# Kernel optimization log

Measured on AMD Instinct MI355X. Metric: run time of the kernel, lower is better.

Reference implementation:

```python
import jax, jax.numpy as jnp
import numpy as np

GRID = 14
N_HEADS = 12
TOP_K = 32


def _valid_indices(grid):
    """Replicates create_locality_mask: cls row/col always valid; patch pairs
    valid iff Chebyshev distance on the grid <= 2 (includes diagonal)."""
    n = grid * grid + 1
    mask = np.zeros((n, n), dtype=bool)
    mask[0, :] = True
    mask[:, 0] = True
    idx = np.arange(grid * grid)
    r, c = idx // grid, idx % grid
    cheb = np.maximum(np.abs(r[:, None] - r[None, :]), np.abs(c[:, None] - c[None, :]))
    mask[1:, 1:] = cheb <= 2
    i_idx, j_idx = np.nonzero(mask)
    return jnp.asarray(i_idx, dtype=jnp.int32), jnp.asarray(j_idx, dtype=jnp.int32)

I_IDX, J_IDX = _valid_indices(GRID)  # nv = 4489 valid (query, key) pairs


def setup_inputs() -> dict:
    key = jax.random.key(0)
    ks = jax.random.split(key, 6)
    B, L, D = 32, GRID * GRID + 1, 768
    s = 0.02
    return {
        "x": jax.random.normal(ks[0], (B, L, D), jnp.float32),
        "W_q": jax.random.normal(ks[1], (D, D), jnp.float32) * s,
        "b_q": jnp.zeros((D,), jnp.float32),
        "W_k": jax.random.normal(ks[2], (D, D), jnp.float32) * s,
        "b_k": jnp.zeros((D,), jnp.float32),
        "W_v": jax.random.normal(ks[3], (D, D), jnp.float32) * s,
        "b_v": jnp.zeros((D,), jnp.float32),
        "W_o": jax.random.normal(ks[4], (D, D), jnp.float32) * s,
        "b_o": jnp.zeros((D,), jnp.float32),
        "log_sigma": jnp.zeros((), jnp.float32),  # sigma = 1.0
    }


def reference(x, W_q, b_q, W_k, b_k, W_v, b_v, W_o, b_o, log_sigma):
    B, L, D = x.shape
    H, dk = N_HEADS, D // N_HEADS

    def proj(W, b):
        y = jnp.einsum('bld,de->ble', x, W) + b
        return y.reshape(B, L, H, dk).transpose(0, 2, 1, 3)  # [B,H,L,dk]

    Q, K, V = proj(W_q, b_q), proj(W_k, b_k), proj(W_v, b_v)

    sigma_sq = jnp.exp(2.0 * log_sigma)
    # gather valid (i,j) pairs; nv pairs from the locality mask
    q_valid = Q[:, :, I_IDX, :]                       # [B,H,nv,dk]
    k_valid = K[:, :, J_IDX, :]                       # [B,H,nv,dk]
    dist_sq = jnp.sum((q_valid - k_valid) ** 2, axis=-1)  # [B,H,nv]
    scores_valid = (-0.5 / sigma_sq) * dist_sq

    neg_inf = jnp.array(-jnp.inf, x.dtype)
    scores = jnp.full((B, H, L, L), neg_inf, dtype=x.dtype)
    scores = scores.at[:, :, I_IDX, J_IDX].set(scores_valid)

    k_top = min(TOP_K, L)
    _, top_idx = jax.lax.top_k(scores, k_top)          # [B,H,L,k]
    bb = jnp.arange(B)[:, None, None, None]
    hh = jnp.arange(H)[None, :, None, None]
    nn = jnp.arange(L)[None, None, :, None]
    topk_mask = jnp.zeros((B, H, L, L), bool).at[bb, hh, nn, top_idx].set(True)

    final_mask = jnp.isfinite(scores) & topk_mask
    scores = jnp.where(final_mask, scores, neg_inf)
    weights = jax.nn.softmax(scores, axis=-1)          # [B,H,L,L]
    attention_mask = (weights > 1e-6).astype(x.dtype)

    consensus = jnp.einsum('bhij,bhjd->bhid', weights, V)
    consensus = consensus.transpose(0, 2, 1, 3).reshape(B, L, D)
    out = jnp.einsum('bld,de->ble', consensus, W_o) + b_o
    return out, weights, attention_mask
```

## Files before the change

### kernel.cpp

```cpp
#include <hip/hip_runtime.h>
#include <hip/hip_bf16.h>
#include <math.h>

#define GRIDN 14
#define L 197
#define H 12
#define DK 64
#define D 768
#define B 32
#define BL (B*L)
#define TOPK 32
#define NBH (B*H)
#define NROW (NBH*L)
#define QKV_ELEMS ((size_t)NROW*DK)
#define KSTR 68
#define KROWS 127

typedef __attribute__((ext_vector_type(8))) short short8;
typedef __attribute__((ext_vector_type(4))) float floatx4;

__device__ __forceinline__ void load_lds16(void* lds, const void* g) {
    __builtin_amdgcn_global_load_lds(
        (const __attribute__((address_space(1))) unsigned int*)g,
        (__attribute__((address_space(3))) unsigned int*)lds, 16, 0, 0);
}

__global__ __launch_bounds__(256)
void prep(const float* __restrict__ x,
          const float* __restrict__ Wq, const float* __restrict__ Wk,
          const float* __restrict__ Wv, const float* __restrict__ Wo,
          __hip_bfloat16* __restrict__ xh, __hip_bfloat16* __restrict__ xl,
          __hip_bfloat16* __restrict__ WqTh, __hip_bfloat16* __restrict__ WqTl,
          __hip_bfloat16* __restrict__ WkTh, __hip_bfloat16* __restrict__ WkTl,
          __hip_bfloat16* __restrict__ WvT,  __hip_bfloat16* __restrict__ WoT)
{
    const int z = blockIdx.z;
    if (z == 4) {
        int lin = (blockIdx.y * 24 + blockIdx.x) * 256 + threadIdx.x;
        for (int i = lin; i < BL * D / 4; i += 24 * 24 * 256) {
            float4 v = ((const float4*)x)[i];
            union { __hip_bfloat16 b[4]; short4 s; } hh, ll;
            float f[4] = {v.x, v.y, v.z, v.w};
            #pragma unroll
            for (int j = 0; j < 4; ++j) {
                __hip_bfloat16 h = __float2bfloat16(f[j]);
                hh.b[j] = h;
                ll.b[j] = __float2bfloat16(f[j] - __bfloat162float(h));
            }
            ((short4*)xh)[i] = hh.s;
            ((short4*)xl)[i] = ll.s;
        }
        return;
    }
    __shared__ float tile[32][33];
    const float* src = (z == 0) ? Wq : (z == 1) ? Wk : (z == 2) ? Wv : Wo;
    __hip_bfloat16* dh = (z == 0) ? WqTh : (z == 1) ? WkTh : (z == 2) ? WvT : WoT;
    __hip_bfloat16* dl = (z == 0) ? WqTl : (z == 1) ? WkTl : nullptr;
    const int k0 = blockIdx.y * 32, n0 = blockIdx.x * 32;
    const int tx = threadIdx.x & 31, ty = threadIdx.x >> 5;

    for (int r = ty; r < 32; r += 8)
        tile[r][tx] = src[(size_t)(k0 + r) * D + n0 + tx];
    __syncthreads();
    for (int r = ty; r < 32; r += 8) {
        float v = tile[tx][r];
        __hip_bfloat16 h = __float2bfloat16(v);
        dh[(size_t)(n0 + r) * D + k0 + tx] = h;
        if (dl) dl[(size_t)(n0 + r) * D + k0 + tx] =
            __float2bfloat16(v - __bfloat162float(h));
    }
}

__global__ __launch_bounds__(256)
void gemm_qkv(const __hip_bfloat16* __restrict__ xh, const __hip_bfloat16* __restrict__ xl,
              const __hip_bfloat16* __restrict__ Wqh, const __hip_bfloat16* __restrict__ Wql,
              const __hip_bfloat16* __restrict__ Wkh, const __hip_bfloat16* __restrict__ Wkl,
              const __hip_bfloat16* __restrict__ Wvh,
              const float* __restrict__ bq, const float* __restrict__ bk,
              const float* __restrict__ bv,
              float* __restrict__ Qb, float* __restrict__ Kb, float* __restrict__ Vb)
{
    __shared__ __attribute__((aligned(16))) __hip_bfloat16 Ash[128 * 32];
    __shared__ __attribute__((aligned(16))) __hip_bfloat16 Bsh[128 * 32];
    __shared__ __attribute__((aligned(16))) __hip_bfloat16 Asl[128 * 32];
    __shared__ __attribute__((aligned(16))) __hip_bfloat16 Bsl[128 * 32];

    const int grp = blockIdx.y / 6, nt = blockIdx.y % 6;
    const __hip_bfloat16 *Bth, *Btl; const float* bias; float* C;
    if (grp == 0)      { Bth = Wqh; Btl = Wql; bias = bq; C = Qb; }
    else if (grp == 1) { Bth = Wkh; Btl = Wkl; bias = bk; C = Kb; }
    else               { Bth = Wvh; Btl = nullptr; bias = bv; C = Vb; }
    const bool split = (grp < 2);

    const int tid = threadIdx.x;
    const int wave = tid >> 6, lane = tid & 63;
    const int quad = lane >> 4, l16 = lane & 15;
    const int m0 = blockIdx.x * 128, n0 = nt * 128;
    const int wm = (wave & 1) * 64, wn = (wave >> 1) * 64;

    floatx4 acc[4][4] = {};

    int s_r[2], s_cs[2];
    #pragma unroll
    for (int u = 0; u < 2; ++u) {
        int idx = tid + u * 256;
        s_r[u] = idx >> 2; s_cs[u] = idx & 3;
    }

    for (int k0 = 0; k0 < D; k0 += 32) {
        #pragma unroll
        for (int u = 0; u < 2; ++u) {
            int r = s_r[u];
            int csrc = s_cs[u] ^ ((r >> 1) & 3);
            int gm = m0 + r; if (gm >= BL) gm = BL - 1;
            size_t aoff = (size_t)gm * D + k0 + csrc * 8;
            size_t boff = (size_t)(n0 + r) * D + k0 + csrc * 8;
            int lds_off = (wave * 64 + u * 256) * 16;
            load_lds16((char*)Ash + lds_off, xh + aoff);
            load_lds16((char*)Bsh + lds_off, Bth + boff);
            if (split) {
                load_lds16((char*)Asl + lds_off, xl + aoff);
                load_lds16((char*)Bsl + lds_off, Btl + boff);
            }
        }
        __syncthreads();

        short8 ah[4], bh[4];
        #pragma unroll
        for (int a = 0; a < 4; ++a) {
            int r = wm + a * 16 + l16;
            int slot = (r << 2) + (quad ^ ((r >> 1) & 3));
            ah[a] = *(const short8*)((const char*)Ash + (slot << 4));
        }
        #pragma unroll
        for (int b2 = 0; b2 < 4; ++b2) {
            int r = wn + b2 * 16 + l16;
            int slot = (r << 2) + (quad ^ ((r >> 1) & 3));
            bh[b2] = *(const short8*)((const char*)Bsh + (slot << 4));
        }
        if (split) {
            short8 al[4], bl[4];
            #pragma unroll
            for (int a = 0; a < 4; ++a) {
                int r = wm + a * 16 + l16;
                int slot = (r << 2) + (quad ^ ((r >> 1) & 3));
                al[a] = *(const short8*)((const char*)Asl + (slot << 4));
            }
            #pragma unroll
            for (int b2 = 0; b2 < 4; ++b2) {
                int r = wn + b2 * 16 + l16;
                int slot = (r << 2) + (quad ^ ((r >> 1) & 3));
                bl[b2] = *(const short8*)((const char*)Bsl + (slot << 4));
            }
            #pragma unroll
            for (int a = 0; a < 4; ++a)
                #pragma unroll
                for (int b2 = 0; b2 < 4; ++b2) {
                    acc[a][b2] = __builtin_amdgcn_mfma_f32_16x16x32_bf16(
                        al[a], bh[b2], acc[a][b2], 0, 0, 0);
                    acc[a][b2] = __builtin_amdgcn_mfma_f32_16x16x32_bf16(
                        ah[a], bl[b2], acc[a][b2], 0, 0, 0);
                }
        }
        #pragma unroll
        for (int a = 0; a < 4; ++a)
            #pragma unroll
            for (int b2 = 0; b2 < 4; ++b2)
                acc[a][b2] = __builtin_amdgcn_mfma_f32_16x16x32_bf16(
                    ah[a], bh[b2], acc[a][b2], 0, 0, 0);
        __syncthreads();
    }

    #pragma unroll
    for (int b2 = 0; b2 < 4; ++b2) {
        int n = n0 + wn + b2 * 16 + l16;
        float bvv = bias[n];
        int hh = n >> 6, dd = n & 63;
        #pragma unroll
        for (int a = 0; a < 4; ++a) {
            #pragma unroll
            for (int r = 0; r < 4; ++r) {
                int m = m0 + wm + a * 16 + quad * 4 + r;
                if (m < BL) {
                    int bb = m / L, ll = m % L;
                    C[((((size_t)bb * H + hh) * L + ll) << 6) + dd] =
                        acc[a][b2][r] + bvv;
                }
            }
        }
    }
}

__global__ __launch_bounds__(256)
void gemm_o(const __hip_bfloat16* __restrict__ A,
            const __hip_bfloat16* __restrict__ Bt,
            const float* __restrict__ bias, float* __restrict__ C)
{
    __shared__ __attribute__((aligned(16))) __hip_bfloat16 As[128 * 32];
    __shared__ __attribute__((aligned(16))) __hip_bfloat16 Bts[128 * 32];

    const int tid = threadIdx.x;
    const int wave = tid >> 6, lane = tid & 63;
    const int quad = lane >> 4, l16 = lane & 15;
    const int m0 = blockIdx.x * 128, n0 = blockIdx.y * 128;
    const int wm = (wave & 1) * 64, wn = (wave >> 1) * 64;

    floatx4 acc[4][4] = {};

    int s_r[2], s_cs[2];
    #pragma unroll
    for (int u = 0; u < 2; ++u) {
        int idx = tid + u * 256;
        s_r[u] = idx >> 2; s_cs[u] = idx & 3;
    }

    for (int k0 = 0; k0 < D; k0 += 32) {
        #pragma unroll
        for (int u = 0; u < 2; ++u) {
            int r = s_r[u];
            int csrc = s_cs[u] ^ ((r >> 1) & 3);
            int gm = m0 + r; if (gm >= BL) gm = BL - 1;
            int lds_off = (wave * 64 + u * 256) * 16;
            load_lds16((char*)As + lds_off, A + (size_t)gm * D + k0 + csrc * 8);
            load_lds16((char*)Bts + lds_off, Bt + (size_t)(n0 + r) * D + k0 + csrc * 8);
        }
        __syncthreads();

        short8 af[4], bf[4];
        #pragma unroll
        for (int a = 0; a < 4; ++a) {
            int r = wm + a * 16 + l16;
            int slot = (r << 2) + (quad ^ ((r >> 1) & 3));
            af[a] = *(const short8*)((const char*)As + (slot << 4));
        }
        #pragma unroll
        for (int b2 = 0; b2 < 4; ++b2) {
            int r = wn + b2 * 16 + l16;
            int slot = (r << 2) + (quad ^ ((r >> 1) & 3));
            bf[b2] = *(const short8*)((const char*)Bts + (slot << 4));
        }
        #pragma unroll
        for (int a = 0; a < 4; ++a)
            #pragma unroll
            for (int b2 = 0; b2 < 4; ++b2)
                acc[a][b2] = __builtin_amdgcn_mfma_f32_16x16x32_bf16(
                    af[a], bf[b2], acc[a][b2], 0, 0, 0);
        __syncthreads();
    }

    #pragma unroll
    for (int b2 = 0; b2 < 4; ++b2) {
        int n = n0 + wn + b2 * 16 + l16;
        float bvv = bias[n];
        #pragma unroll
        for (int a = 0; a < 4; ++a) {
            #pragma unroll
            for (int r = 0; r < 4; ++r) {
                int m = m0 + wm + a * 16 + quad * 4 + r;
                if (m < BL) C[(size_t)m * D + n] = acc[a][b2][r] + bvv;
            }
        }
    }
}

__global__ __launch_bounds__(512)
void attn_fused(const float* __restrict__ Q, const float* __restrict__ Kg,
                const float* __restrict__ Vg, const float* __restrict__ logsig,
                float* __restrict__ wout, float* __restrict__ mout,
                __hip_bfloat16* __restrict__ cons)
{
    __shared__ __attribute__((aligned(16))) float KV[KROWS * KSTR];
    __shared__ float qbuf[8][64];
    __shared__ float clsbuf[L];
    __shared__ float wjW[99][32];
    __shared__ unsigned char wjJ[99][32];
    __shared__ unsigned int winA[L];
    __shared__ unsigned char joff[76];

    const int bh = blockIdx.x;
    const int yb = blockIdx.y;
    const int b = bh / H, h = bh % H;
    const int tid = threadIdx.x, wave = tid >> 6, lane = tid & 63;
    const int base_i = yb * 99;
    const int half = lane & 1;
    const int joffs = yb ? 70 : 0;

    if (tid >= 1 && tid < L) {
        int r = (tid - 1) / GRIDN, c = (tid - 1) % GRIDN;
        int r0 = r - 2 < 0 ? 0 : r - 2, r1 = r + 2 > 13 ? 13 : r + 2;
        int c0 = c - 2 < 0 ? 0 : c - 2, c1 = c + 2 > 13 ? 13 : c + 2;
        int Wd = c1 - c0 + 1, Hh = r1 - r0 + 1;
        winA[tid] = (unsigned)r0 | ((unsigned)c0 << 8) |
                    ((unsigned)Wd << 16) | ((unsigned)Hh << 24);
    }
    if (tid == 0) winA[0] = 0;
    if (tid < 75) {
        int w = tid / 25 + 3, tm = tid % 25;
        joff[tid] = (unsigned char)((tm / w) * GRIDN + tm % w);
    }

    int pr4[4], pc4[4];
    #pragma unroll
    for (int k = 0; k < 4; ++k) {
        int p = lane + (k << 6);
        if (p >= 1 && p < L) { pr4[k] = (p - 1) / GRIDN; pc4[k] = (p - 1) % GRIDN; }
        else                 { pr4[k] = 255; pc4[k] = 255; }
    }

    const float* Kp = Kg + (size_t)bh * L * DK;
    for (int idx = tid; idx < KROWS * 16; idx += 512) {
        int r = idx >> 4, c4 = idx & 15;
        int g = r ? r + joffs : 0;
        *(float4*)&KV[r * KSTR + c4 * 4] = *(const float4*)&Kp[g * 64 + c4 * 4];
    }
    __syncthreads();

    const float coef = -0.5f * expf(-2.0f * logsig[0]);
    const int starts0[9] = {0, 9, 22, 35, 48, 61, 74, 87, 99};
    const int starts1[9] = {99, 112, 124, 136, 148, 161, 173, 185, 197};
    const int i_begin = yb ? starts1[wave] : starts0[wave];
    const int i_end   = yb ? starts1[wave + 1] : starts0[wave + 1];

    float qreg = (i_begin < i_end)
               ? Q[((size_t)bh * L + i_begin) * 64 + lane] : 0.f;

    for (int i = i_begin; i < i_end; ++i) {
        const int rowid = bh * L + i;
        const size_t wb = (size_t)rowid * L;
        const int local = i - base_i;

        qbuf[wave][lane] = qreg;
        if (i + 1 < i_end)
            qreg = Q[((size_t)rowid + 1) * 64 + lane];

        if (i == 0) {
            const float4* qp = (const float4*)&qbuf[wave][half << 5];
            for (int p = 0; p < 7; ++p) {
                int t = (p << 5) + (lane >> 1);
                bool valid = t < L;
                float s = 0.f;
                if (valid) {
                    const float4* kp = (const float4*)&Kp[(size_t)t * DK + (half << 5)];
                    #pragma unroll
                    for (int d4 = 0; d4 < 8; ++d4) {
                        float4 qv = qp[d4], kv = kp[d4];
                        float dx = qv.x - kv.x, dy = qv.y - kv.y;
                        float dz = qv.z - kv.z, dw = qv.w - kv.w;
                        s += dx * dx + dy * dy + dz * dz + dw * dw;
                    }
                }
                s += __shfl_xor(s, 1);
                if (valid && !half) clsbuf[t] = coef * s;
            }
            float orig[4], cur[4]; int selb = 0;
            #pragma unroll
            for (int k = 0; k < 4; ++k) {
                int t = lane + (k << 6);
                float v = (t < L) ? clsbuf[t] : -INFINITY;
                orig[k] = v; cur[k] = v;
            }
            float gmax = -INFINITY;
            for (int it = 0; it < TOPK; ++it) {
                float bv = cur[0]; int bt = lane;
                #pragma unroll
                for (int k = 1; k < 4; ++k)
                    if (cur[k] > bv) { bv = cur[k]; bt = lane + (k << 6); }
                #pragma unroll
                for (int off = 32; off; off >>= 1) {
                    float ov = __shfl_xor(bv, off);
                    int   ot = __shfl_xor(bt, off);
                    if (ov > bv || (ov == bv && ot < bt)) { bv = ov; bt = ot; }
                }
                if (it == 0) gmax = bv;
                if ((bt & 63) == lane) { cur[bt >> 6] = -INFINITY; selb |= 1 << (bt >> 6); }
            }
            float zl = 0.f; float wk[4];
            #pragma unroll
            for (int k = 0; k < 4; ++k) {
                wk[k] = ((selb >> k) & 1) ? expf(orig[k] - gmax) : 0.f;
                zl += wk[k];
            }
            #pragma unroll
            for (int off = 32; off; off >>= 1) zl += __shfl_xor(zl, off);

            #pragma unroll
            for (int k = 0; k < 4; ++k) {
                int p = lane + (k << 6);
                if (p < L) {
                    float wv = wk[k] / zl;
                    wout[wb + p] = wv;
                    mout[wb + p] = (wv > 1e-6f) ? 1.f : 0.f;
                }
            }
            int slot = 0;
            #pragma unroll
            for (int k = 0; k < 4; ++k) {
                bool sel = (selb >> k) & 1;
                unsigned long long mk = __ballot(sel);
                if (sel) {
                    int tt = slot + (int)__popcll(mk & ((1ull << lane) - 1ull));
                    wjW[0][tt] = wk[k] / zl;
                    wjJ[0][tt] = (unsigned char)(lane + (k << 6));
                }
                slot += (int)__popcll(mk);
            }
        } else {
            const unsigned wa = winA[i];
            const int r0 = wa & 255, c0 = (wa >> 8) & 255;
            const int Wd2 = (wa >> 16) & 255, Hh = wa >> 24;
            const int n = Hh * Wd2 + 1;
            const int jbase = 1 + r0 * GRIDN + c0;

            int t = lane >> 1;
            bool valid = t < n;
            float s = 0.f; int j = 0;
            if (valid) {
                if (t > 0) j = jbase + joff[(Wd2 - 3) * 25 + (t - 1)];
                int js = j ? j - joffs : 0;
                const float4* kp = (const float4*)&KV[js * KSTR + (half << 5)];
                const float4* qp = (const float4*)&qbuf[wave][half << 5];
                #pragma unroll
                for (int d4 = 0; d4 < 8; ++d4) {
                    float4 qv = qp[d4], kv = kp[d4];
                    float dx = qv.x - kv.x, dy = qv.y - kv.y;
                    float dz = qv.z - kv.z, dw = qv.w - kv.w;
                    s += dx * dx + dy * dy + dz * dz + dw * dw;
                }
                j = js;
            }
            s += __shfl_xor(s, 1);
            float sc = valid ? coef * s : -INFINITY;

            float mx = sc;
            #pragma unroll
            for (int off = 32; off; off >>= 1) mx = fmaxf(mx, __shfl_xor(mx, off));
            float e = valid ? expf(sc - mx) : 0.f;
            float es = half ? 0.f : e;
            #pragma unroll
            for (int off = 32; off; off >>= 1) es += __shfl_xor(es, off);
            float wv = e / es;

            if (!half) {
                float wcv = valid ? wv : 0.f;
                wjW[local][t] = wcv;
                wjJ[local][t] = (unsigned char)(valid ? j : 0);
            }
            #pragma unroll
            for (int k = 0; k < 4; ++k) {
                int p = lane + (k << 6);
                if (p < L) {
                    float wd = 0.f;
                    if (p == 0) wd = wjW[local][0];
                    else {
                        unsigned du = (unsigned)(pr4[k] - r0);
                        unsigned dv = (unsigned)(pc4[k] - c0);
                        if (du < (unsigned)Hh && dv < (unsigned)Wd2)
                            wd = wjW[local][1 + du * Wd2 + dv];
                    }
                    wout[wb + p] = wd;
                    mout[wb + p] = (wd > 1e-6f) ? 1.f : 0.f;
                }
            }
        }
    }
    __syncthreads();

    const float* Vp = Vg + (size_t)bh * L * DK;
    for (int idx = tid; idx < KROWS * 16; idx += 512) {
        int r = idx >> 4, c4 = idx & 15;
        int g = r ? r + joffs : 0;
        *(float4*)&KV[r * KSTR + c4 * 4] = *(const float4*)&Vp[g * 64 + c4 * 4];
    }
    __syncthreads();

    const int cstarts0[9] = {0, 13, 26, 38, 50, 62, 74, 87, 99};
    const int c_begin = yb ? starts1[wave] : cstarts0[wave];
    const int c_end   = yb ? starts1[wave + 1] : cstarts0[wave + 1];

    for (int i = c_begin; i < c_end; ++i) {
        const int local = i - base_i;
        float acc = 0.f;
        if (i == 0) {
            #pragma unroll
            for (int t = 0; t < 32; ++t) {
                float w = wjW[0][t];
                int j = wjJ[0][t];
                acc += w * Vp[(size_t)j * DK + lane];
            }
        } else {
            #pragma unroll
            for (int t = 0; t < 32; ++t) {
                float w = wjW[local][t];
                int j = wjJ[local][t];
                acc += w * KV[j * KSTR + lane];
            }
        }
        cons[((size_t)b * L + i) * D + h * 64 + lane] = __float2bfloat16(acc);
    }
}

extern "C" void kernel_launch(void* const* d_in, const int* in_sizes, int n_in,
                              void* d_out, int out_size, void* d_ws, size_t ws_size,
                              hipStream_t stream)
{
    const float* x   = (const float*)d_in[0];
    const float* Wq  = (const float*)d_in[1];
    const float* bq  = (const float*)d_in[2];
    const float* Wk  = (const float*)d_in[3];
    const float* bk  = (const float*)d_in[4];
    const float* Wv  = (const float*)d_in[5];
    const float* bv  = (const float*)d_in[6];
    const float* Wo  = (const float*)d_in[7];
    const float* bo  = (const float*)d_in[8];
    const float* lsg = (const float*)d_in[9];

    float* out  = (float*)d_out;
    float* wout = out + QKV_ELEMS;
    float* mout = wout + (size_t)B * H * L * L;

    float* Qb  = (float*)d_ws;
    float* Kb  = Qb + QKV_ELEMS;
    float* Vb  = Kb + QKV_ELEMS;
    __hip_bfloat16* xh = (__hip_bfloat16*)(Vb + QKV_ELEMS);
    __hip_bfloat16* xl = xh + (size_t)BL * D;
    __hip_bfloat16* WqTh = xl + (size_t)BL * D;
    __hip_bfloat16* WqTl = WqTh + (size_t)D * D;
    __hip_bfloat16* WkTh = WqTl + (size_t)D * D;
    __hip_bfloat16* WkTl = WkTh + (size_t)D * D;
    __hip_bfloat16* WvT  = WkTl + (size_t)D * D;
    __hip_bfloat16* WoT  = WvT  + (size_t)D * D;
    __hip_bfloat16* consb = xh;

    prep<<<dim3(24, 24, 5), 256, 0, stream>>>(
        x, Wq, Wk, Wv, Wo, xh, xl, WqTh, WqTl, WkTh, WkTl, WvT, WoT);

    gemm_qkv<<<dim3(50, 18), 256, 0, stream>>>(
        xh, xl, WqTh, WqTl, WkTh, WkTl, WvT, bq, bk, bv, Qb, Kb, Vb);

    attn_fused<<<dim3(NBH, 2), 512, 0, stream>>>(
        Qb, Kb, Vb, lsg, wout, mout, consb);

    gemm_o<<<dim3(50, 6), 256, 0, stream>>>(consb, WoT, bo, out);
}
```

Measured before the change: 383.0 us.

## Split CLS-row attention into separate kernel to remove divergent branch

The CLS query row, which needs a full 197-key scan and a top-32 selection, moves out of the fused attention kernel into its own small kernel with one 64-thread block per (batch, head). The patch kernel then handles only rows 1..196, so the i==0 branches in both the score and consensus loops go away and the work split across waves is rebalanced. This removes the load imbalance where one wave in each y=0 block carried the expensive CLS row. The cost is an extra kernel launch plus a tiny, low-occupancy kernel that runs serially before the patch kernel.

```diff
diff --git a/kernel.cpp b/kernel.cpp
--- a/kernel.cpp
+++ b/kernel.cpp
@@ -263,15 +263,118 @@
     }
 }
 
+__global__ __launch_bounds__(64)
+void attn_cls(const float* __restrict__ Q, const float* __restrict__ Kg,
+              const float* __restrict__ Vg, const float* __restrict__ logsig,
+              float* __restrict__ wout, float* __restrict__ mout,
+              __hip_bfloat16* __restrict__ cons)
+{
+    __shared__ float qbuf[64];
+    __shared__ float clsbuf[L];
+    __shared__ float w0[32];
+    __shared__ unsigned char j0[32];
+
+    const int bh = blockIdx.x;
+    const int b = bh / H, h = bh % H;
+    const int lane = threadIdx.x;
+    const int half = lane & 1;
+    const float* Kp = Kg + (size_t)bh * L * DK;
+    const float* Vp = Vg + (size_t)bh * L * DK;
+    const size_t wb = (size_t)(bh * L) * L;
+
+    qbuf[lane] = Q[(size_t)bh * L * DK + lane];
+    const float coef = -0.5f * expf(-2.0f * logsig[0]);
+    __syncthreads();
+
+    const float4* qp = (const float4*)&qbuf[half << 5];
+    for (int p = 0; p < 7; ++p) {
+        int t = (p << 5) + (lane >> 1);
+        bool valid = t < L;
+        float s = 0.f;
+        if (valid) {
+            const float4* kp = (const float4*)&Kp[(size_t)t * DK + (half << 5)];
+            #pragma unroll
+            for (int d4 = 0; d4 < 8; ++d4) {
+                float4 qv = qp[d4], kv = kp[d4];
+                float dx = qv.x - kv.x, dy = qv.y - kv.y;
+                float dz = qv.z - kv.z, dw = qv.w - kv.w;
+                s += dx * dx + dy * dy + dz * dz + dw * dw;
+            }
+        }
+        s += __shfl_xor(s, 1);
+        if (valid && !half) clsbuf[t] = coef * s;
+    }
+    __syncthreads();
+
+    float orig[4], cur[4]; int selb = 0;
+    #pragma unroll
+    for (int k = 0; k < 4; ++k) {
+        int t = lane + (k << 6);
+        float v = (t < L) ? clsbuf[t] : -INFINITY;
+        orig[k] = v; cur[k] = v;
+    }
+    float gmax = -INFINITY;
+    for (int it = 0; it < TOPK; ++it) {
+        float bv = cur[0]; int bt = lane;
+        #pragma unroll
+        for (int k = 1; k < 4; ++k)
+            if (cur[k] > bv) { bv = cur[k]; bt = lane + (k << 6); }
+        #pragma unroll
+        for (int off = 32; off; off >>= 1) {
+            float ov = __shfl_xor(bv, off);
+            int   ot = __shfl_xor(bt, off);
+            if (ov > bv || (ov == bv && ot < bt)) { bv = ov; bt = ot; }
+        }
+        if (it == 0) gmax = bv;
+        if ((bt & 63) == lane) { cur[bt >> 6] = -INFINITY; selb |= 1 << (bt >> 6); }
+    }
+    float zl = 0.f; float wk[4];
+    #pragma unroll
+    for (int k = 0; k < 4; ++k) {
+        wk[k] = ((selb >> k) & 1) ? expf(orig[k] - gmax) : 0.f;
+        zl += wk[k];
+    }
+    #pragma unroll
+    for (int off = 32; off; off >>= 1) zl += __shfl_xor(zl, off);
+
+    #pragma unroll
+    for (int k = 0; k < 4; ++k) {
+        int p = lane + (k << 6);
+        if (p < L) {
+            float wv = wk[k] / zl;
+            wout[wb + p] = wv;
+            mout[wb + p] = (wv > 1e-6f) ? 1.f : 0.f;
+        }
+    }
+    int slot = 0;
+    #pragma unroll
+    for (int k = 0; k < 4; ++k) {
+        bool sel = (selb >> k) & 1;
+        unsigned long long mk = __ballot(sel);
+        if (sel) {
+            int tt = slot + (int)__popcll(mk & ((1ull << lane) - 1ull));
+            w0[tt] = wk[k] / zl;
+            j0[tt] = (unsigned char)(lane + (k << 6));
+        }
+        slot += (int)__popcll(mk);
+    }
+    __syncthreads();
+
+    float acc = 0.f;
+    #pragma unroll
+    for (int t = 0; t < 32; ++t)
+        acc += w0[t] * Vp[(size_t)j0[t] * DK + lane];
+    cons[((size_t)b * L) * D + h * 64 + lane] = __float2bfloat16(acc);
+}
+
 __global__ __launch_bounds__(512)
-void attn_fused(const float* __restrict__ Q, const float* __restrict__ Kg,
+void attn_patch(const float* __restrict__ Q, const float* __restrict__ Kg,
                 const float* __restrict__ Vg, const float* __restrict__ logsig,
                 float* __restrict__ wout, float* __restrict__ mout,
                 __hip_bfloat16* __restrict__ cons)
 {
     __shared__ __attribute__((aligned(16))) float KV[KROWS * KSTR];
     __shared__ float qbuf[8][64];
-    __shared__ float clsbuf[L];
     __shared__ float wjW[99][32];
     __shared__ unsigned char wjJ[99][32];
     __shared__ unsigned int winA[L];
@@ -293,7 +396,6 @@
         winA[tid] = (unsigned)r0 | ((unsigned)c0 << 8) |
                     ((unsigned)Wd << 16) | ((unsigned)Hh << 24);
     }
-    if (tid == 0) winA[0] = 0;
     if (tid < 75) {
         int w = tid / 25 + 3, tm = tid % 25;
         joff[tid] = (unsigned char)((tm / w) * GRIDN + tm % w);
@@ -316,7 +418,7 @@
     __syncthreads();
 
     const float coef = -0.5f * expf(-2.0f * logsig[0]);
-    const int starts0[9] = {0, 9, 22, 35, 48, 61, 74, 87, 99};
+    const int starts0[9] = {1, 14, 27, 39, 51, 63, 75, 87, 99};
     const int starts1[9] = {99, 112, 124, 136, 148, 161, 173, 185, 197};
     const int i_begin = yb ? starts1[wave] : starts0[wave];
     const int i_end   = yb ? starts1[wave + 1] : starts0[wave + 1];
@@ -333,133 +435,60 @@
         if (i + 1 < i_end)
             qreg = Q[((size_t)rowid + 1) * 64 + lane];
 
-        if (i == 0) {
+        const unsigned wa = winA[i];
+        const int r0 = wa & 255, c0 = (wa >> 8) & 255;
+        const int Wd2 = (wa >> 16) & 255, Hh = wa >> 24;
+        const int n = Hh * Wd2 + 1;
+        const int jbase = 1 + r0 * GRIDN + c0;
+
+        int t = lane >> 1;
+        bool valid = t < n;
+        float s = 0.f; int j = 0;
+        if (valid) {
+            if (t > 0) j = jbase + joff[(Wd2 - 3) * 25 + (t - 1)];
+            int js = j ? j - joffs : 0;
+            const float4* kp = (const float4*)&KV[js * KSTR + (half << 5)];
             const float4* qp = (const float4*)&qbuf[wave][half << 5];
-            for (int p = 0; p < 7; ++p) {
-                int t = (p << 5) + (lane >> 1);
-                bool valid = t < L;
-                float s = 0.f;
-                if (valid) {
-                    const float4* kp = (const float4*)&Kp[(size_t)t * DK + (half << 5)];
-                    #pragma unroll
-                    for (int d4 = 0; d4 < 8; ++d4) {
-                        float4 qv = qp[d4], kv = kp[d4];
-                        float dx = qv.x - kv.x, dy = qv.y - kv.y;
-                        float dz = qv.z - kv.z, dw = qv.w - kv.w;
-                        s += dx * dx + dy * dy + dz * dz + dw * dw;
-                    }
+            #pragma unroll
+            for (int d4 = 0; d4 < 8; ++d4) {
+                float4 qv = qp[d4], kv = kp[d4];
+                float dx = qv.x - kv.x, dy = qv.y - kv.y;
+                float dz = qv.z - kv.z, dw = qv.w - kv.w;
+                s += dx * dx + dy * dy + dz * dz + dw * dw;
+            }
+            j = js;
+        }
+        s += __shfl_xor(s, 1);
+        float sc = valid ? coef * s : -INFINITY;
+
+        float mx = sc;
+        #pragma unroll
+        for (int off = 32; off; off >>= 1) mx = fmaxf(mx, __shfl_xor(mx, off));
+        float e = valid ? expf(sc - mx) : 0.f;
+        float es = half ? 0.f : e;
+        #pragma unroll
+        for (int off = 32; off; off >>= 1) es += __shfl_xor(es, off);
+        float wv = e / es;
+
+        if (!half) {
+            float wcv = valid ? wv : 0.f;
+            wjW[local][t] = wcv;
+            wjJ[local][t] = (unsigned char)(valid ? j : 0);
+        }
+        #pragma unroll
+        for (int k = 0; k < 4; ++k) {
+            int p = lane + (k << 6);
+            if (p < L) {
+                float wd = 0.f;
+                if (p == 0) wd = wjW[local][0];
+                else {
+                    unsigned du = (unsigned)(pr4[k] - r0);
+                    unsigned dv = (unsigned)(pc4[k] - c0);
+                    if (du < (unsigned)Hh && dv < (unsigned)Wd2)
+                        wd = wjW[local][1 + du * Wd2 + dv];
                 }
-                s += __shfl_xor(s, 1);
-                if (valid && !half) clsbuf[t] = coef * s;
-            }
-            float orig[4], cur[4]; int selb = 0;
-            #pragma unroll
-            for (int k = 0; k < 4; ++k) {
-                int t = lane + (k << 6);
-                float v = (t < L) ? clsbuf[t] : -INFINITY;
-                orig[k] = v; cur[k] = v;
-            }
-            float gmax = -INFINITY;
-            for (int it = 0; it < TOPK; ++it) {
-                float bv = cur[0]; int bt = lane;
-                #pragma unroll
-                for (int k = 1; k < 4; ++k)
-                    if (cur[k] > bv) { bv = cur[k]; bt = lane + (k << 6); }
-                #pragma unroll
-                for (int off = 32; off; off >>= 1) {
-                    float ov = __shfl_xor(bv, off);
-                    int   ot = __shfl_xor(bt, off);
-                    if (ov > bv || (ov == bv && ot < bt)) { bv = ov; bt = ot; }
-                }
-                if (it == 0) gmax = bv;
-                if ((bt & 63) == lane) { cur[bt >> 6] = -INFINITY; selb |= 1 << (bt >> 6); }
-            }
-            float zl = 0.f; float wk[4];
-            #pragma unroll
-            for (int k = 0; k < 4; ++k) {
-                wk[k] = ((selb >> k) & 1) ? expf(orig[k] - gmax) : 0.f;
-                zl += wk[k];
-            }
-            #pragma unroll
-            for (int off = 32; off; off >>= 1) zl += __shfl_xor(zl, off);
-
-            #pragma unroll
-            for (int k = 0; k < 4; ++k) {
-                int p = lane + (k << 6);
-                if (p < L) {
-                    float wv = wk[k] / zl;
-                    wout[wb + p] = wv;
-                    mout[wb + p] = (wv > 1e-6f) ? 1.f : 0.f;
-                }
-            }
-            int slot = 0;
-            #pragma unroll
-            for (int k = 0; k < 4; ++k) {
-                bool sel = (selb >> k) & 1;
-                unsigned long long mk = __ballot(sel);
-                if (sel) {
-                    int tt = slot + (int)__popcll(mk & ((1ull << lane) - 1ull));
-                    wjW[0][tt] = wk[k] / zl;
-                    wjJ[0][tt] = (unsigned char)(lane + (k << 6));
-                }
-                slot += (int)__popcll(mk);
-            }
-        } else {
-            const unsigned wa = winA[i];
-            const int r0 = wa & 255, c0 = (wa >> 8) & 255;
-            const int Wd2 = (wa >> 16) & 255, Hh = wa >> 24;
-            const int n = Hh * Wd2 + 1;
-            const int jbase = 1 + r0 * GRIDN + c0;
-
-            int t = lane >> 1;
-            bool valid = t < n;
-            float s = 0.f; int j = 0;
-            if (valid) {
-                if (t > 0) j = jbase + joff[(Wd2 - 3) * 25 + (t - 1)];
-                int js = j ? j - joffs : 0;
-                const float4* kp = (const float4*)&KV[js * KSTR + (half << 5)];
-                const float4* qp = (const float4*)&qbuf[wave][half << 5];
-                #pragma unroll
-                for (int d4 = 0; d4 < 8; ++d4) {
-                    float4 qv = qp[d4], kv = kp[d4];
-                    float dx = qv.x - kv.x, dy = qv.y - kv.y;
-                    float dz = qv.z - kv.z, dw = qv.w - kv.w;
-                    s += dx * dx + dy * dy + dz * dz + dw * dw;
-                }
-                j = js;
-            }
-            s += __shfl_xor(s, 1);
-            float sc = valid ? coef * s : -INFINITY;
-
-            float mx = sc;
-            #pragma unroll
-            for (int off = 32; off; off >>= 1) mx = fmaxf(mx, __shfl_xor(mx, off));
-            float e = valid ? expf(sc - mx) : 0.f;
-            float es = half ? 0.f : e;
-            #pragma unroll
-            for (int off = 32; off; off >>= 1) es += __shfl_xor(es, off);
-            float wv = e / es;
-
-            if (!half) {
-                float wcv = valid ? wv : 0.f;
-                wjW[local][t] = wcv;
-                wjJ[local][t] = (unsigned char)(valid ? j : 0);
-            }
-            #pragma unroll
-            for (int k = 0; k < 4; ++k) {
-                int p = lane + (k << 6);
-                if (p < L) {
-                    float wd = 0.f;
-                    if (p == 0) wd = wjW[local][0];
-                    else {
-                        unsigned du = (unsigned)(pr4[k] - r0);
-                        unsigned dv = (unsigned)(pc4[k] - c0);
-                        if (du < (unsigned)Hh && dv < (unsigned)Wd2)
-                            wd = wjW[local][1 + du * Wd2 + dv];
-                    }
-                    wout[wb + p] = wd;
-                    mout[wb + p] = (wd > 1e-6f) ? 1.f : 0.f;
-                }
+                wout[wb + p] = wd;
+                mout[wb + p] = (wd > 1e-6f) ? 1.f : 0.f;
             }
         }
     }
@@ -473,27 +502,17 @@
     }
     __syncthreads();
 
-    const int cstarts0[9] = {0, 13, 26, 38, 50, 62, 74, 87, 99};
-    const int c_begin = yb ? starts1[wave] : cstarts0[wave];
-    const int c_end   = yb ? starts1[wave + 1] : cstarts0[wave + 1];
+    const int c_begin = yb ? starts1[wave] : starts0[wave];
+    const int c_end   = yb ? starts1[wave + 1] : starts0[wave + 1];
 
     for (int i = c_begin; i < c_end; ++i) {
         const int local = i - base_i;
         float acc = 0.f;
-        if (i == 0) {
-            #pragma unroll
-            for (int t = 0; t < 32; ++t) {
-                float w = wjW[0][t];
-                int j = wjJ[0][t];
-                acc += w * Vp[(size_t)j * DK + lane];
-            }
-        } else {
-            #pragma unroll
-            for (int t = 0; t < 32; ++t) {
-                float w = wjW[local][t];
-                int j = wjJ[local][t];
-                acc += w * KV[j * KSTR + lane];
-            }
+        #pragma unroll
+        for (int t = 0; t < 32; ++t) {
+            float w = wjW[local][t];
+            int j = wjJ[local][t];
+            acc += w * KV[j * KSTR + lane];
         }
         cons[((size_t)b * L + i) * D + h * 64 + lane] = __float2bfloat16(acc);
     }
@@ -537,8 +556,11 @@
     gemm_qkv<<<dim3(50, 18), 256, 0, stream>>>(
         xh, xl, WqTh, WqTl, WkTh, WkTl, WvT, bq, bk, bv, Qb, Kb, Vb);
 
-    attn_fused<<<dim3(NBH, 2), 512, 0, stream>>>(
+    attn_cls<<<dim3(NBH), 64, 0, stream>>>(
         Qb, Kb, Vb, lsg, wout, mout, consb);
 
+    attn_patch<<<dim3(NBH, 2), 512, 0, stream>>>(
+        Qb, Kb, Vb, lsg, wout, mout, consb);
+
     gemm_o<<<dim3(50, 6), 256, 0, stream>>>(consb, WoT, bo, out);
 }
```

New measurement: 349.2 us. -8.8%, faster.
